# Kernel tuning notes

Measured on AMD Instinct MI355X. Metric: run time of the kernel, lower is better.

Reference implementation:

```python
import jax, jax.numpy as jnp
import numpy as np

B, LQ, LKV, C, H, Z = 4, 1024, 4096, 256, 8, 1024


def setup_inputs() -> dict:
    key = jax.random.key(0)
    ks = jax.random.split(key, 10)
    s = 0.02  # small init scale for weights
    return {
        "q": jax.random.normal(ks[0], (B, LQ, C), jnp.float32),
        "kv": jax.random.normal(ks[1], (B, LKV, C), jnp.float32),
        "q_ape": jax.random.normal(ks[2], (1, LQ, C), jnp.float32),
        "k_ape": jax.random.normal(ks[3], (1, LKV - Z, C), jnp.float32),
        "attn_pos": jax.random.normal(ks[4], (1, H, LQ, Z), jnp.float32),
        "Wq": jax.random.normal(ks[5], (C, C), jnp.float32) * s,
        "Wk": jax.random.normal(ks[6], (C, C), jnp.float32) * s,
        "Wv": jax.random.normal(ks[7], (C, C), jnp.float32) * s,
        "Wp": jax.random.normal(ks[8], (C, C), jnp.float32) * s,
        "bp": jnp.zeros((C,), jnp.float32),
        "z_shape": Z,
    }


def reference(q, kv, q_ape, k_ape, attn_pos, Wq, Wk, Wv, Wp, bp, z_shape):
    Bn, Lq, Cd = q.shape
    d = Cd // H
    scale = d ** (-0.5)
    # q path: APE added before projection
    qh = ((q + q_ape) @ Wq.T).reshape(Bn, Lq, H, d).transpose(0, 2, 1, 3)  # (B,H,Lq,d)
    # in-place `k[:, z_shape:, :] += k_ape` in torch aliases kv, so v also sees it
    kvm = kv.at[:, z_shape:, :].add(k_ape)
    kh = (kvm @ Wk.T).reshape(Bn, -1, H, d).transpose(0, 2, 1, 3)  # (B,H,Lkv,d)
    vh = (kvm @ Wv.T).reshape(Bn, -1, H, d).transpose(0, 2, 1, 3)  # (B,H,Lkv,d)
    attn = jnp.einsum('bhqd,bhkd->bhqk', qh, kh) * scale           # (B,H,Lq,Lkv)
    # partial positional bias on the template slice only
    attn = attn.at[:, :, :, :z_shape].add(attn_pos)
    attn = jax.nn.softmax(attn, axis=-1)
    x = jnp.einsum('bhqk,bhkd->bhqd', attn, vh)
    x = x.transpose(0, 2, 1, 3).reshape(Bn, Lq, Cd)
    return x @ Wp.T + bp
```

## Files before the change

kernel.cpp:

```cpp
#include <hip/hip_runtime.h>


typedef __attribute__((ext_vector_type(8))) short bf16x8;
typedef __attribute__((ext_vector_type(4))) float f32x4;
typedef __attribute__((ext_vector_type(4))) unsigned short u16x4;

#define MFMA16(a, b, c) __builtin_amdgcn_mfma_f32_16x16x32_bf16((a), (b), (c), 0, 0, 0)

__device__ __forceinline__ unsigned short f2bf(float f) {
  return __builtin_bit_cast(unsigned short, static_cast<__bf16>(f));
}
__device__ __forceinline__ float bf2f(unsigned short u) {
  return __builtin_bit_cast(float, ((unsigned)u) << 16);
}

__global__ __launch_bounds__(256) void prep_all(const float* __restrict__ Wq,
                                                const float* __restrict__ Wk,
                                                const float* __restrict__ Wv,
                                                const float* __restrict__ Wp,
                                                const float* __restrict__ pos,
                                                const float* __restrict__ Xq,
                                                const float* __restrict__ Xkv,
                                                const float* __restrict__ q_ape,
                                                const float* __restrict__ k_ape,
                                                unsigned short* __restrict__ wout,
                                                unsigned short* __restrict__ pfb,
                                                unsigned short* __restrict__ kvp,
                                                unsigned short* __restrict__ qp,
                                                int posBlocks) {
  int bx = blockIdx.x;
  if (bx < posBlocks) {
    const int s4 = bx * 256 + threadIdx.x;
    const int zk4 = s4 & 255, q = (s4 >> 8) & 1023, h = s4 >> 18;
    const float4 v = *(const float4*)(pos + ((size_t)s4 << 2));
    const int kt = zk4 >> 4, c = (zk4 >> 2) & 3, g = zk4 & 3;
    const float L = 1.4426950408889634f;
    u16x4 o = { f2bf(v.x * L), f2bf(v.y * L), f2bf(v.z * L), f2bf(v.w * L) };
    *(u16x4*)(pfb + (size_t)((h << 6) + (q >> 4)) * 16384 + ((kt << 2) + c) * 256 + ((q & 15) << 4) + (g << 2)) = o;
    return;
  }
  bx -= posBlocks;
  if (bx < 128) {
    const int idx = bx * 256 + threadIdx.x;
    const int which = idx >> 13, rem = idx & 8191;
    const int o = rem >> 5, colb = (rem & 31) << 3;
    const float* src = (which == 0) ? Wq : (which == 1) ? Wk : (which == 2) ? Wv : Wp;
    float4 v0 = *(const float4*)(src + (size_t)o * 256 + colb);
    float4 v1 = *(const float4*)(src + (size_t)o * 256 + colb + 4);
    if (which == 0) {
      const float qs = 0.17677669529663687f * 1.4426950408889634f;
      v0.x *= qs; v0.y *= qs; v0.z *= qs; v0.w *= qs;
      v1.x *= qs; v1.y *= qs; v1.z *= qs; v1.w *= qs;
    }
    const int n = o >> 4, x = o & 15, k = colb >> 5, g = (colb & 31) >> 3;
    unsigned short* dst = wout + (which << 16) + n * 4096 + k * 512 + x * 32 + g * 8;
    u16x4 a = { f2bf(v0.x), f2bf(v0.y), f2bf(v0.z), f2bf(v0.w) };
    u16x4 b = { f2bf(v1.x), f2bf(v1.y), f2bf(v1.z), f2bf(v1.w) };
    *(u16x4*)dst = a;
    *(u16x4*)(dst + 4) = b;
    return;
  }
  bx -= 128;
  if (bx < 2048) {
    const int idx = bx * 256 + threadIdx.x;
    const int row = idx >> 5, c8 = idx & 31;
    const int col = c8 << 3, lq = row & 4095;
    const float* xp = Xkv + (size_t)row * 256 + col;
    float4 v0 = *(const float4*)xp, v1 = *(const float4*)(xp + 4);
    if (lq >= 1024) {
      const float* ap = k_ape + (size_t)(lq - 1024) * 256 + col;
      const float4 a0 = *(const float4*)ap, a1 = *(const float4*)(ap + 4);
      v0.x += a0.x; v0.y += a0.y; v0.z += a0.z; v0.w += a0.w;
      v1.x += a1.x; v1.y += a1.y; v1.z += a1.z; v1.w += a1.w;
    }
    const int k = c8 >> 2, g = c8 & 3;
    unsigned short* dst = kvp + (size_t)(row >> 4) * 4096 + k * 512 + (row & 15) * 32 + g * 8;
    u16x4 a = { f2bf(v0.x), f2bf(v0.y), f2bf(v0.z), f2bf(v0.w) };
    u16x4 b = { f2bf(v1.x), f2bf(v1.y), f2bf(v1.z), f2bf(v1.w) };
    *(u16x4*)dst = a;
    *(u16x4*)(dst + 4) = b;
    return;
  }
  bx -= 2048;
  {
    const int idx = bx * 256 + threadIdx.x;
    const int row = idx >> 5, c8 = idx & 31;
    const int col = c8 << 3, arow = row & 1023;
    const float* xp = Xq + (size_t)row * 256 + col;
    const float* ap = q_ape + (size_t)arow * 256 + col;
    const float4 v0 = *(const float4*)xp, v1 = *(const float4*)(xp + 4);
    const float4 a0 = *(const float4*)ap, a1 = *(const float4*)(ap + 4);
    const int k = c8 >> 2, g = c8 & 3;
    unsigned short* dst = qp + (size_t)(row >> 4) * 4096 + k * 512 + (row & 15) * 32 + g * 8;
    u16x4 a = { f2bf(v0.x + a0.x), f2bf(v0.y + a0.y), f2bf(v0.z + a0.z), f2bf(v0.w + a0.w) };
    u16x4 b = { f2bf(v1.x + a1.x), f2bf(v1.y + a1.y), f2bf(v1.z + a1.z), f2bf(v1.w + a1.w) };
    *(u16x4*)dst = a;
    *(u16x4*)(dst + 4) = b;
  }
}

__global__ __launch_bounds__(256, 4) void proj_qkv(const unsigned short* __restrict__ kvp,
                                                   const unsigned short* __restrict__ qp,
                                                   const unsigned short* __restrict__ Wqb,
                                                   const unsigned short* __restrict__ Wkb,
                                                   const unsigned short* __restrict__ Wvb,
                                                   unsigned short* __restrict__ Qhp,
                                                   unsigned short* __restrict__ Khp,
                                                   unsigned short* __restrict__ Vsp) {
  const int tid = threadIdx.x;
  const int w = tid >> 6, lane = tid & 63, x = lane & 15, g = lane >> 4;
  const int rg = w & 1, nh = w >> 1;
  const int bx = blockIdx.x;
  if (bx < 1024) {
    const bool isV = bx >= 512;
    const int bk = isV ? bx - 512 : bx;
    const int rbase = bk * 32 + rg * 16;
    const unsigned short* ap = kvp + (size_t)(rbase >> 4) * 4096 + x * 32 + g * 8;
    bf16x8 a[8];
#pragma unroll
    for (int k = 0; k < 8; ++k) a[k] = *(const bf16x8*)(ap + k * 512);
    const unsigned short* Wb = isV ? Wvb : Wkb;
    f32x4 acc[8];
#pragma unroll
    for (int n = 0; n < 8; ++n) acc[n] = (f32x4){0.f, 0.f, 0.f, 0.f};
#pragma unroll
    for (int k = 0; k < 8; ++k)
#pragma unroll
      for (int n0 = 0; n0 < 8; ++n0) {
        const bf16x8 bw = *(const bf16x8*)(Wb + (size_t)(nh * 8 + n0) * 4096 + k * 512 + x * 32 + g * 8);
        acc[n0] = MFMA16(a[k], bw, acc[n0]);
      }
    if (!isV) {
      const int b2 = rbase >> 12, kk0 = (rbase & 4095) + g * 4;
#pragma unroll
      for (int n0 = 0; n0 < 8; ++n0) {
        const int n = nh * 8 + n0, hh = n >> 1, dd = ((n & 1) << 4) + x;
        unsigned short* kp = Khp + (size_t)(b2 * 8 + hh) * 131072;
#pragma unroll
        for (int r = 0; r < 4; ++r)
          kp[(size_t)(kk0 + r) * 32 + dd] = f2bf(acc[n0][r]);
      }
    } else {
      const int b2 = rbase >> 12, T = (rbase >> 6) & 63, c0 = (rbase >> 4) & 3;
      const int ks = c0 & 1, ih = (c0 >> 1) << 2;
#pragma unroll
      for (int n0 = 0; n0 < 8; ++n0) {
        const int n = nh * 8 + n0, hh = n >> 1, dh = n & 1;
        u16x4 o = { f2bf(acc[n0][0]), f2bf(acc[n0][1]), f2bf(acc[n0][2]), f2bf(acc[n0][3]) };
        *(u16x4*)(Vsp + (size_t)(b2 * 8 + hh) * 131072 + T * 2048 + ks * 1024 + dh * 512 + g * 128 + x * 8 + ih) = o;
      }
    }
  } else {
    const int bq = bx - 1024;
    const int rbase = bq * 32 + rg * 16;
    const unsigned short* ap = qp + (size_t)(rbase >> 4) * 4096 + x * 32 + g * 8;
    bf16x8 a[8];
#pragma unroll
    for (int k = 0; k < 8; ++k) a[k] = *(const bf16x8*)(ap + k * 512);
    f32x4 acc[8];
#pragma unroll
    for (int n = 0; n < 8; ++n) acc[n] = (f32x4){0.f, 0.f, 0.f, 0.f};
#pragma unroll
    for (int k = 0; k < 8; ++k)
#pragma unroll
      for (int n0 = 0; n0 < 8; ++n0) {
        const bf16x8 bw = *(const bf16x8*)(Wqb + (size_t)(nh * 8 + n0) * 4096 + k * 512 + x * 32 + g * 8);
        acc[n0] = MFMA16(a[k], bw, acc[n0]);
      }
    const int b2 = rbase >> 10, qr0 = (rbase & 1023) + g * 4;
#pragma unroll
    for (int n0 = 0; n0 < 8; ++n0) {
      const int n = nh * 8 + n0, hh = n >> 1, dd = ((n & 1) << 4) + x;
      unsigned short* qpn = Qhp + (size_t)(b2 * 8 + hh) * 32768;
#pragma unroll
      for (int r = 0; r < 4; ++r)
        qpn[(size_t)(qr0 + r) * 32 + dd] = f2bf(acc[n0][r]);
    }
  }
}

template <int SPLIT, bool PF>
__global__ __launch_bounds__(256, 4) void
attn_fused(const unsigned short* __restrict__ Qhp,
           const unsigned short* __restrict__ Khp,
           const unsigned short* __restrict__ Vsp,
           const void* __restrict__ pos,
           unsigned short* __restrict__ Xo,
           float* __restrict__ Opart,
           float* __restrict__ lpart) {
  const int tid = threadIdx.x;
  const int w = tid >> 6, lane = tid & 63, x = lane & 15, g = lane >> 4;
  const int bid = blockIdx.x;
  const int h = bid & 7, b = (bid >> 3) & 3, qt = (bid >> 5) & 7, z = bid >> 8;
  const int qrow0 = qt * 128 + w * 32;
  const int NT = 64 / SPLIT;

  const unsigned short* Qpl = Qhp + (size_t)(b * 8 + h) * 32768;
  const bf16x8 aq0 = *(const bf16x8*)(Qpl + (size_t)(qrow0 + x) * 32 + g * 8);
  const bf16x8 aq1 = *(const bf16x8*)(Qpl + (size_t)(qrow0 + 16 + x) * 32 + g * 8);
  const unsigned short* Kpl = Khp + (size_t)(b * 8 + h) * 131072 + x * 32 + g * 8;
  const unsigned short* Vpl = Vsp + (size_t)(b * 8 + h) * 131072 + g * 128 + x * 8;
  const unsigned short* pq0 = PF ? (const unsigned short*)pos + (size_t)((h << 6) + (qt << 3) + (w << 1)) * 16384 : nullptr;
  const unsigned short* pq1 = PF ? pq0 + 16384 : nullptr;
  const float* pr0 = PF ? nullptr : (const float*)pos + (size_t)((h << 10) + qrow0 + x) * 1024;
  const float* pr1 = PF ? nullptr : (const float*)pos + (size_t)((h << 10) + qrow0 + 16 + x) * 1024;
  const f32x4 zc = {0.f, 0.f, 0.f, 0.f};

  f32x4 o00 = zc, o01 = zc, o10 = zc, o11 = zc;
  float ls0 = 0.f, ls1 = 0.f;

  bf16x8 ka[4], va[4];
#pragma unroll
  for (int c = 0; c < 4; ++c)
    ka[c] = *(const bf16x8*)(Kpl + (size_t)((z << 6) + c * 16) * 32);
#pragma unroll
  for (int j = 0; j < 4; ++j)
    va[j] = *(const bf16x8*)(Vpl + (z << 11) + (j << 9));

#define GROUP(AQ, PQ, PR, LS, OA, OB, T, BIAS)                                               \
  do {                                                                                       \
    f32x4 s[4];                                                                              \
    _Pragma("unroll")                                                                        \
    for (int c = 0; c < 4; ++c) s[c] = MFMA16(ka[c], AQ, zc);                                \
    if (BIAS) {                                                                              \
      if (PF) {                                                                              \
        _Pragma("unroll")                                                                    \
        for (int c = 0; c < 4; ++c) {                                                        \
          const u16x4 p = *(const u16x4*)(PQ + ((T) << 10) + (c << 8) + (x << 4) + (g << 2)); \
          s[c][0] += bf2f(p[0]); s[c][1] += bf2f(p[1]);                                      \
          s[c][2] += bf2f(p[2]); s[c][3] += bf2f(p[3]);                                      \
        }                                                                                    \
      } else {                                                                               \
        const float LOG2E = 1.4426950408889634f;                                             \
        _Pragma("unroll")                                                                    \
        for (int c = 0; c < 4; ++c) {                                                        \
          const float4 p = *(const float4*)(PR + ((T) << 6) + c * 16 + g * 4);               \
          s[c][0] = fmaf(p.x, LOG2E, s[c][0]); s[c][1] = fmaf(p.y, LOG2E, s[c][1]);          \
          s[c][2] = fmaf(p.z, LOG2E, s[c][2]); s[c][3] = fmaf(p.w, LOG2E, s[c][3]);          \
        }                                                                                    \
      }                                                                                      \
    }                                                                                        \
    _Pragma("unroll")                                                                        \
    for (int c = 0; c < 4; ++c)                                                              \
      _Pragma("unroll")                                                                      \
      for (int r = 0; r < 4; ++r) {                                                          \
        s[c][r] = __builtin_amdgcn_exp2f(s[c][r]); LS += s[c][r];                            \
      }                                                                                      \
    bf16x8 pa0, pa1;                                                                         \
    _Pragma("unroll")                                                                        \
    for (int r = 0; r < 4; ++r) {                                                            \
      pa0[r] = (short)f2bf(s[0][r]); pa0[4 + r] = (short)f2bf(s[2][r]);                      \
      pa1[r] = (short)f2bf(s[1][r]); pa1[4 + r] = (short)f2bf(s[3][r]);                      \
    }                                                                                        \
    OA = MFMA16(pa0, va[0], OA); OB = MFMA16(pa0, va[1], OB);                                \
    OA = MFMA16(pa1, va[2], OA); OB = MFMA16(pa1, va[3], OB);                                \
  } while (0)

#define TILE(T, BIAS)                                                                        \
  do {                                                                                       \
    const int tp = ((T) + SPLIT <= 63) ? (T) + SPLIT : (T);                                  \
    GROUP(aq0, pq0, pr0, ls0, o00, o01, T, BIAS);                                            \
    GROUP(aq1, pq1, pr1, ls1, o10, o11, T, BIAS);                                            \
    _Pragma("unroll")                                                                        \
    for (int c = 0; c < 4; ++c)                            \
      ka[c] = *(const bf16x8*)(Kpl + (size_t)((tp << 6) + c * 16) * 32);                     \
    _Pragma("unroll")                                                                        \
    for (int j = 0; j < 4; ++j)                            \
      va[j] = *(const bf16x8*)(Vpl + (tp << 11) + (j << 9));                                 \
  } while (0)

  const int nb = 16 / SPLIT;
  int t = z;
  for (int i = 0; i < nb; ++i) { TILE(t, true);  t += SPLIT; }
  for (int i = nb; i < NT; ++i) { TILE(t, false); t += SPLIT; }
#undef TILE
#undef GROUP

  ls0 += __shfl_xor(ls0, 16); ls0 += __shfl_xor(ls0, 32);
  ls1 += __shfl_xor(ls1, 16); ls1 += __shfl_xor(ls1, 32);

  if (SPLIT == 1) {
    const float inv0 = 1.f / ls0, inv1 = 1.f / ls1;
    const int rowblk = (b << 6) + (qt << 3) + (w << 1);
#pragma unroll
    for (int r = 0; r < 4; ++r) {
      const float ir0 = __shfl(inv0, g * 4 + r, 64);
      const float ir1 = __shfl(inv1, g * 4 + r, 64);
      unsigned short* d0 = Xo + (size_t)rowblk * 4096 + h * 512 + (g * 4 + r) * 32;
      unsigned short* d1 = Xo + (size_t)(rowblk + 1) * 4096 + h * 512 + (g * 4 + r) * 32;
      d0[x] = f2bf(o00[r] * ir0);
      d0[16 + x] = f2bf(o01[r] * ir0);
      d1[x] = f2bf(o10[r] * ir1);
      d1[16 + x] = f2bf(o11[r] * ir1);
    }
  } else {
    if (g == 0) {
      __builtin_nontemporal_store(ls0, &lpart[(size_t)z * 32768 + ((b << 10) + qrow0 + x) * 8 + h]);
      __builtin_nontemporal_store(ls1, &lpart[(size_t)z * 32768 + ((b << 10) + qrow0 + 16 + x) * 8 + h]);
    }
#pragma unroll
    for (int r = 0; r < 4; ++r) {
      const size_t orow0 = (size_t)z * 1048576 + (size_t)((b << 10) + qrow0 + g * 4 + r) * 256 + h * 32;
      const size_t orow1 = (size_t)z * 1048576 + (size_t)((b << 10) + qrow0 + 16 + g * 4 + r) * 256 + h * 32;
      __builtin_nontemporal_store(o00[r], &Opart[orow0 + x]);
      __builtin_nontemporal_store(o01[r], &Opart[orow0 + 16 + x]);
      __builtin_nontemporal_store(o10[r], &Opart[orow1 + x]);
      __builtin_nontemporal_store(o11[r], &Opart[orow1 + 16 + x]);
    }
  }
}

__global__ __launch_bounds__(256) void combine(const float* __restrict__ Opart,
                                               const float* __restrict__ lpart,
                                               unsigned short* __restrict__ Xo, int split) {
  const int idx = blockIdx.x * 256 + threadIdx.x;
  const int row = idx >> 6, c4 = (idx & 63) << 2, h = c4 >> 5;
  float l = 0.f;
  float4 o = {0.f, 0.f, 0.f, 0.f};
  for (int zz = 0; zz < split; ++zz) {
    l += lpart[(size_t)zz * 32768 + row * 8 + h];
    const float4 ov = *(const float4*)(Opart + (size_t)zz * 1048576 + (size_t)row * 256 + c4);
    o.x += ov.x; o.y += ov.y; o.z += ov.z; o.w += ov.w;
  }
  const float inv = 1.f / l;
  u16x4 pk = { f2bf(o.x * inv), f2bf(o.y * inv), f2bf(o.z * inv), f2bf(o.w * inv) };
  unsigned short* dst = Xo + (size_t)(row >> 4) * 4096 + h * 512 +
                        (row & 15) * 32 + ((c4 >> 3) & 3) * 8 + (c4 & 7);
  *(u16x4*)dst = pk;
}

__global__ __launch_bounds__(256) void proj_out(const unsigned short* __restrict__ Xp,
                                                const unsigned short* __restrict__ Wb,
                                                const float* __restrict__ bias,
                                                float* __restrict__ out) {
  const int tid = threadIdx.x;
  const int w = tid >> 6, lane = tid & 63, x = lane & 15, g = lane >> 4;
  const int rbase = blockIdx.x << 4;
  const int cb = w << 6;
  const unsigned short* ap = Xp + (size_t)blockIdx.x * 4096 + x * 32 + g * 8;
  bf16x8 a[8];
#pragma unroll
  for (int k = 0; k < 8; ++k) a[k] = *(const bf16x8*)(ap + k * 512);
  f32x4 acc[4];
#pragma unroll
  for (int n = 0; n < 4; ++n) acc[n] = (f32x4){0.f, 0.f, 0.f, 0.f};
#pragma unroll
  for (int k = 0; k < 8; ++k)
#pragma unroll
    for (int n = 0; n < 4; ++n) {
      const bf16x8 bw = *(const bf16x8*)(Wb + (size_t)((w << 2) + n) * 4096 + k * 512 + x * 32 + g * 8);
      acc[n] = MFMA16(a[k], bw, acc[n]);
    }
#pragma unroll
  for (int n = 0; n < 4; ++n) {
    const float bv = bias[cb + n * 16 + x];
#pragma unroll
    for (int r = 0; r < 4; ++r)
      out[(size_t)(rbase + g * 4 + r) * 256 + cb + n * 16 + x] = acc[n][r] + bv;
  }
}

extern "C" void kernel_launch(void* const* d_in, const int* in_sizes, int n_in,
                              void* d_out, int out_size, void* d_ws, size_t ws_size,
                              hipStream_t stream) {
  const float* q        = (const float*)d_in[0];
  const float* kv       = (const float*)d_in[1];
  const float* q_ape    = (const float*)d_in[2];
  const float* k_ape    = (const float*)d_in[3];
  const float* attn_pos = (const float*)d_in[4];
  const float* Wq       = (const float*)d_in[5];
  const float* Wk       = (const float*)d_in[6];
  const float* Wv       = (const float*)d_in[7];
  const float* Wp       = (const float*)d_in[8];
  const float* bp       = (const float*)d_in[9];
  float* out = (float*)d_out;

  unsigned short* wsb = (unsigned short*)d_ws;
  unsigned short* Wqb = wsb;
  unsigned short* Wkb = wsb + 65536;
  unsigned short* Wvb = wsb + 131072;
  unsigned short* Wpb = wsb + 196608;
  unsigned short* Qhp = wsb + 262144;
  unsigned short* Khp = wsb + 1310720;
  unsigned short* Vsp = wsb + 5505024;
  unsigned short* Xws = wsb + 9699328;
  unsigned short* kvp = wsb + 10747904;
  unsigned short* qp  = wsb + 14942208;

  const size_t L0  = 31981568ull;
  const size_t PFB = 16777216ull;
  const size_t PS  = 4325376ull;
  int split; bool havepf;
  if      (ws_size >= L0 + PFB + 4 * PS) { split = 4; havepf = true; }
  else if (ws_size >= L0 + 4 * PS)       { split = 4; havepf = false; }
  else if (ws_size >= L0 + 2 * PS)       { split = 2; havepf = false; }
  else                                   { split = 1; havepf = false; }
  unsigned short* pfb = (unsigned short*)((char*)d_ws + L0);
  float* Opart = (float*)((char*)d_ws + L0 + (havepf ? PFB : 0));
  float* lpart = Opart + (size_t)split * 1048576;

  const int posBlocks = havepf ? 8192 : 0;
  prep_all<<<posBlocks + 128 + 2048 + 512, 256, 0, stream>>>(
      Wq, Wk, Wv, Wp, attn_pos, q, kv, q_ape, k_ape, wsb, pfb, kvp, qp, posBlocks);
  proj_qkv<<<1152, 256, 0, stream>>>(kvp, qp, Wqb, Wkb, Wvb, Qhp, Khp, Vsp);
  if (havepf)
    attn_fused<4, true><<<1024, 256, 0, stream>>>(Qhp, Khp, Vsp, pfb, Xws, Opart, lpart);
  else if (split == 4)
    attn_fused<4, false><<<1024, 256, 0, stream>>>(Qhp, Khp, Vsp, attn_pos, Xws, Opart, lpart);
  else if (split == 2)
    attn_fused<2, false><<<512, 256, 0, stream>>>(Qhp, Khp, Vsp, attn_pos, Xws, Opart, lpart);
  else
    attn_fused<1, false><<<256, 256, 0, stream>>>(Qhp, Khp, Vsp, attn_pos, Xws, Opart, lpart);
  if (split > 1) combine<<<1024, 256, 0, stream>>>(Opart, lpart, Xws, split);
  proj_out<<<256, 256, 0, stream>>>(Xws, Wpb, bp, out);
}
```

Before: 88.47 us.

## Fuse split-KV combine into output projection and raise KV split to eight

```diff
diff --git a/kernel.cpp b/kernel.cpp
--- a/kernel.cpp
+++ b/kernel.cpp
@@ -298,35 +298,76 @@
       __builtin_nontemporal_store(ls0, &lpart[(size_t)z * 32768 + ((b << 10) + qrow0 + x) * 8 + h]);
       __builtin_nontemporal_store(ls1, &lpart[(size_t)z * 32768 + ((b << 10) + qrow0 + 16 + x) * 8 + h]);
     }
+    const int rowblk = (b << 6) + (qt << 3) + (w << 1);
 #pragma unroll
     for (int r = 0; r < 4; ++r) {
-      const size_t orow0 = (size_t)z * 1048576 + (size_t)((b << 10) + qrow0 + g * 4 + r) * 256 + h * 32;
-      const size_t orow1 = (size_t)z * 1048576 + (size_t)((b << 10) + qrow0 + 16 + g * 4 + r) * 256 + h * 32;
-      __builtin_nontemporal_store(o00[r], &Opart[orow0 + x]);
-      __builtin_nontemporal_store(o01[r], &Opart[orow0 + 16 + x]);
-      __builtin_nontemporal_store(o10[r], &Opart[orow1 + x]);
-      __builtin_nontemporal_store(o11[r], &Opart[orow1 + 16 + x]);
-    }
-  }
-}
-
-__global__ __launch_bounds__(256) void combine(const float* __restrict__ Opart,
-                                               const float* __restrict__ lpart,
-                                               unsigned short* __restrict__ Xo, int split) {
-  const int idx = blockIdx.x * 256 + threadIdx.x;
-  const int row = idx >> 6, c4 = (idx & 63) << 2, h = c4 >> 5;
-  float l = 0.f;
-  float4 o = {0.f, 0.f, 0.f, 0.f};
+      float* b0 = Opart + (size_t)z * 1048576 + (size_t)rowblk * 4096 + h * 512 + (g * 4 + r) * 32;
+      float* b1 = b0 + 4096;
+      __builtin_nontemporal_store(o00[r], b0 + x);
+      __builtin_nontemporal_store(o01[r], b0 + 16 + x);
+      __builtin_nontemporal_store(o10[r], b1 + x);
+      __builtin_nontemporal_store(o11[r], b1 + 16 + x);
+    }
+  }
+}
+
+__global__ __launch_bounds__(256) void proj_out_c(const float* __restrict__ Opart,
+                                                  const float* __restrict__ lpart,
+                                                  const unsigned short* __restrict__ Wb,
+                                                  const float* __restrict__ bias,
+                                                  float* __restrict__ out, int split) {
+  const int tid = threadIdx.x;
+  const int w = tid >> 6, lane = tid & 63, x = lane & 15, g = lane >> 4;
+  const int blk = blockIdx.x, rbase = blk << 4;
+  const int cb = w << 6;
+
+  float l[8];
+#pragma unroll
+  for (int k = 0; k < 8; ++k) l[k] = 0.f;
   for (int zz = 0; zz < split; ++zz) {
-    l += lpart[(size_t)zz * 32768 + row * 8 + h];
-    const float4 ov = *(const float4*)(Opart + (size_t)zz * 1048576 + (size_t)row * 256 + c4);
-    o.x += ov.x; o.y += ov.y; o.z += ov.z; o.w += ov.w;
-  }
-  const float inv = 1.f / l;
-  u16x4 pk = { f2bf(o.x * inv), f2bf(o.y * inv), f2bf(o.z * inv), f2bf(o.w * inv) };
-  unsigned short* dst = Xo + (size_t)(row >> 4) * 4096 + h * 512 +
-                        (row & 15) * 32 + ((c4 >> 3) & 3) * 8 + (c4 & 7);
-  *(u16x4*)dst = pk;
+    const float* lp = lpart + (size_t)zz * 32768 + (size_t)(rbase + x) * 8;
+    const float4 l0 = *(const float4*)lp, l1 = *(const float4*)(lp + 4);
+    l[0] += l0.x; l[1] += l0.y; l[2] += l0.z; l[3] += l0.w;
+    l[4] += l1.x; l[5] += l1.y; l[6] += l1.z; l[7] += l1.w;
+  }
+#pragma unroll
+  for (int k = 0; k < 8; ++k) l[k] = 1.f / l[k];
+
+  bf16x8 a[8];
+#pragma unroll
+  for (int k = 0; k < 8; ++k) {
+    float s[8];
+#pragma unroll
+    for (int i = 0; i < 8; ++i) s[i] = 0.f;
+    for (int zz = 0; zz < split; ++zz) {
+      const float* op = Opart + (size_t)zz * 1048576 + (size_t)blk * 4096 + k * 512 + x * 32 + g * 8;
+      const float4 v0 = *(const float4*)op, v1 = *(const float4*)(op + 4);
+      s[0] += v0.x; s[1] += v0.y; s[2] += v0.z; s[3] += v0.w;
+      s[4] += v1.x; s[5] += v1.y; s[6] += v1.z; s[7] += v1.w;
+    }
+    bf16x8 av;
+#pragma unroll
+    for (int i = 0; i < 8; ++i) av[i] = (short)f2bf(s[i] * l[k]);
+    a[k] = av;
+  }
+
+  f32x4 acc[4];
+#pragma unroll
+  for (int n = 0; n < 4; ++n) acc[n] = (f32x4){0.f, 0.f, 0.f, 0.f};
+#pragma unroll
+  for (int k = 0; k < 8; ++k)
+#pragma unroll
+    for (int n = 0; n < 4; ++n) {
+      const bf16x8 bw = *(const bf16x8*)(Wb + (size_t)((w << 2) + n) * 4096 + k * 512 + x * 32 + g * 8);
+      acc[n] = MFMA16(a[k], bw, acc[n]);
+    }
+#pragma unroll
+  for (int n = 0; n < 4; ++n) {
+    const float bv = bias[cb + n * 16 + x];
+#pragma unroll
+    for (int r = 0; r < 4; ++r)
+      out[(size_t)(rbase + g * 4 + r) * 256 + cb + n * 16 + x] = acc[n][r] + bv;
+  }
 }
 
 __global__ __launch_bounds__(256) void proj_out(const unsigned short* __restrict__ Xp,
@@ -391,7 +432,8 @@
   const size_t PFB = 16777216ull;
   const size_t PS  = 4325376ull;
   int split; bool havepf;
-  if      (ws_size >= L0 + PFB + 4 * PS) { split = 4; havepf = true; }
+  if      (ws_size >= L0 + PFB + 8 * PS) { split = 8; havepf = true; }
+  else if (ws_size >= L0 + PFB + 4 * PS) { split = 4; havepf = true; }
   else if (ws_size >= L0 + 4 * PS)       { split = 4; havepf = false; }
   else if (ws_size >= L0 + 2 * PS)       { split = 2; havepf = false; }
   else                                   { split = 1; havepf = false; }
@@ -403,7 +445,9 @@
   prep_all<<<posBlocks + 128 + 2048 + 512, 256, 0, stream>>>(
       Wq, Wk, Wv, Wp, attn_pos, q, kv, q_ape, k_ape, wsb, pfb, kvp, qp, posBlocks);
   proj_qkv<<<1152, 256, 0, stream>>>(kvp, qp, Wqb, Wkb, Wvb, Qhp, Khp, Vsp);
-  if (havepf)
+  if (havepf && split == 8)
+    attn_fused<8, true><<<2048, 256, 0, stream>>>(Qhp, Khp, Vsp, pfb, Xws, Opart, lpart);
+  else if (havepf)
     attn_fused<4, true><<<1024, 256, 0, stream>>>(Qhp, Khp, Vsp, pfb, Xws, Opart, lpart);
   else if (split == 4)
     attn_fused<4, false><<<1024, 256, 0, stream>>>(Qhp, Khp, Vsp, attn_pos, Xws, Opart, lpart);
@@ -411,6 +455,8 @@
     attn_fused<2, false><<<512, 256, 0, stream>>>(Qhp, Khp, Vsp, attn_pos, Xws, Opart, lpart);
   else
     attn_fused<1, false><<<256, 256, 0, stream>>>(Qhp, Khp, Vsp, attn_pos, Xws, Opart, lpart);
-  if (split > 1) combine<<<1024, 256, 0, stream>>>(Opart, lpart, Xws, split);
-  proj_out<<<256, 256, 0, stream>>>(Xws, Wpb, bp, out);
-}
+  if (split > 1)
+    proj_out_c<<<256, 256, 0, stream>>>(Opart, lpart, Wpb, bp, out, split);
+  else
+    proj_out<<<256, 256, 0, stream>>>(Xws, Wpb, bp, out);
+}
```

Measured after the change: 120.5 us. 1.36x slower.

## Stage K/V tiles in double-buffered LDS shared across attention waves

Applied to the files above, without the earlier changes.

```diff
diff --git a/kernel.cpp b/kernel.cpp
--- a/kernel.cpp
+++ b/kernel.cpp
@@ -131,14 +131,17 @@
         acc[n0] = MFMA16(a[k], bw, acc[n0]);
       }
     if (!isV) {
-      const int b2 = rbase >> 12, kk0 = (rbase & 4095) + g * 4;
+      const int b2 = rbase >> 12;
+      const int T2 = (rbase & 4095) >> 6, c2 = (rbase >> 4) & 3;
 #pragma unroll
       for (int n0 = 0; n0 < 8; ++n0) {
-        const int n = nh * 8 + n0, hh = n >> 1, dd = ((n & 1) << 4) + x;
-        unsigned short* kp = Khp + (size_t)(b2 * 8 + hh) * 131072;
+        const int n = nh * 8 + n0, hh = n >> 1;
+        const int g2 = ((n & 1) << 1) + (x >> 3), i2 = x & 7;
+        unsigned short* kp = Khp + (size_t)(b2 * 8 + hh) * 131072 +
+                             T2 * 2048 + (c2 * 4 + g2) * 128 + i2;
 #pragma unroll
         for (int r = 0; r < 4; ++r)
-          kp[(size_t)(kk0 + r) * 32 + dd] = f2bf(acc[n0][r]);
+          kp[(g * 4 + r) * 8] = f2bf(acc[n0][r]);
       }
     } else {
       const int b2 = rbase >> 12, T = (rbase >> 6) & 63, c0 = (rbase >> 4) & 3;
@@ -188,6 +191,8 @@
            unsigned short* __restrict__ Xo,
            float* __restrict__ Opart,
            float* __restrict__ lpart) {
+  __shared__ unsigned short ldsK[2][2048];
+  __shared__ unsigned short ldsV[2][2048];
   const int tid = threadIdx.x;
   const int w = tid >> 6, lane = tid & 63, x = lane & 15, g = lane >> 4;
   const int bid = blockIdx.x;
@@ -198,8 +203,9 @@
   const unsigned short* Qpl = Qhp + (size_t)(b * 8 + h) * 32768;
   const bf16x8 aq0 = *(const bf16x8*)(Qpl + (size_t)(qrow0 + x) * 32 + g * 8);
   const bf16x8 aq1 = *(const bf16x8*)(Qpl + (size_t)(qrow0 + 16 + x) * 32 + g * 8);
-  const unsigned short* Kpl = Khp + (size_t)(b * 8 + h) * 131072 + x * 32 + g * 8;
-  const unsigned short* Vpl = Vsp + (size_t)(b * 8 + h) * 131072 + g * 128 + x * 8;
+  const unsigned short* Ksrc = Khp + (size_t)(b * 8 + h) * 131072;
+  const unsigned short* Vsrc = Vsp + (size_t)(b * 8 + h) * 131072;
+  const int stageoff = w * 512 + lane * 8;
   const unsigned short* pq0 = PF ? (const unsigned short*)pos + (size_t)((h << 6) + (qt << 3) + (w << 1)) * 16384 : nullptr;
   const unsigned short* pq1 = PF ? pq0 + 16384 : nullptr;
   const float* pr0 = PF ? nullptr : (const float*)pos + (size_t)((h << 10) + qrow0 + x) * 1024;
@@ -209,15 +215,15 @@
   f32x4 o00 = zc, o01 = zc, o10 = zc, o11 = zc;
   float ls0 = 0.f, ls1 = 0.f;
 
-  bf16x8 ka[4], va[4];
-#pragma unroll
-  for (int c = 0; c < 4; ++c)
-    ka[c] = *(const bf16x8*)(Kpl + (size_t)((z << 6) + c * 16) * 32);
-#pragma unroll
-  for (int j = 0; j < 4; ++j)
-    va[j] = *(const bf16x8*)(Vpl + (z << 11) + (j << 9));
-
-#define GROUP(AQ, PQ, PR, LS, OA, OB, T, BIAS)                                               \
+  {
+    const bf16x8 kq = *(const bf16x8*)(Ksrc + (z << 11) + stageoff);
+    const bf16x8 vq = *(const bf16x8*)(Vsrc + (z << 11) + stageoff);
+    *(bf16x8*)(&ldsK[0][stageoff]) = kq;
+    *(bf16x8*)(&ldsV[0][stageoff]) = vq;
+  }
+  __syncthreads();
+
+#define GROUP(AQ, PQ, PR, LS, OA, OB, T, BIAS, CUR)                                          \
   do {                                                                                       \
     f32x4 s[4];                                                                              \
     _Pragma("unroll")                                                                        \
@@ -252,27 +258,38 @@
       pa0[r] = (short)f2bf(s[0][r]); pa0[4 + r] = (short)f2bf(s[2][r]);                      \
       pa1[r] = (short)f2bf(s[1][r]); pa1[4 + r] = (short)f2bf(s[3][r]);                      \
     }                                                                                        \
-    OA = MFMA16(pa0, va[0], OA); OB = MFMA16(pa0, va[1], OB);                                \
-    OA = MFMA16(pa1, va[2], OA); OB = MFMA16(pa1, va[3], OB);                                \
+    OA = MFMA16(pa0, *(const bf16x8*)(&ldsV[CUR][g * 128 + x * 8]), OA);                     \
+    OB = MFMA16(pa0, *(const bf16x8*)(&ldsV[CUR][512 + g * 128 + x * 8]), OB);               \
+    OA = MFMA16(pa1, *(const bf16x8*)(&ldsV[CUR][1024 + g * 128 + x * 8]), OA);              \
+    OB = MFMA16(pa1, *(const bf16x8*)(&ldsV[CUR][1536 + g * 128 + x * 8]), OB);              \
   } while (0)
 
-#define TILE(T, BIAS)                                                                        \
+#define TILE(T, BIAS, CUR)                                                                   \
   do {                                                                                       \
     const int tp = ((T) + SPLIT <= 63) ? (T) + SPLIT : (T);                                  \
-    GROUP(aq0, pq0, pr0, ls0, o00, o01, T, BIAS);                                            \
-    GROUP(aq1, pq1, pr1, ls1, o10, o11, T, BIAS);                                            \
+    const bf16x8 kq = *(const bf16x8*)(Ksrc + (tp << 11) + stageoff);                        \
+    const bf16x8 vq = *(const bf16x8*)(Vsrc + (tp << 11) + stageoff);                        \
+    bf16x8 ka[4];                                                                            \
     _Pragma("unroll")                                                                        \
-    for (int c = 0; c < 4; ++c)                            \
-      ka[c] = *(const bf16x8*)(Kpl + (size_t)((tp << 6) + c * 16) * 32);                     \
-    _Pragma("unroll")                                                                        \
-    for (int j = 0; j < 4; ++j)                            \
-      va[j] = *(const bf16x8*)(Vpl + (tp << 11) + (j << 9));                                 \
+    for (int c = 0; c < 4; ++c)                                                              \
+      ka[c] = *(const bf16x8*)(&ldsK[CUR][(c * 4 + g) * 128 + x * 8]);                       \
+    GROUP(aq0, pq0, pr0, ls0, o00, o01, T, BIAS, CUR);                                       \
+    GROUP(aq1, pq1, pr1, ls1, o10, o11, T, BIAS, CUR);                                       \
+    *(bf16x8*)(&ldsK[(CUR) ^ 1][stageoff]) = kq;                                             \
+    *(bf16x8*)(&ldsV[(CUR) ^ 1][stageoff]) = vq;                                             \
+    __syncthreads();                                                                         \
   } while (0)
 
   const int nb = 16 / SPLIT;
   int t = z;
-  for (int i = 0; i < nb; ++i) { TILE(t, true);  t += SPLIT; }
-  for (int i = nb; i < NT; ++i) { TILE(t, false); t += SPLIT; }
+  for (int i = 0; i < nb; i += 2) {
+    TILE(t, true, 0);  t += SPLIT;
+    TILE(t, true, 1);  t += SPLIT;
+  }
+  for (int i = nb; i < NT; i += 2) {
+    TILE(t, false, 0); t += SPLIT;
+    TILE(t, false, 1); t += SPLIT;
+  }
 #undef TILE
 #undef GROUP
 
```

Measured after the change: 83.86 us, median of 2. 1.05x faster.
